# Kernel tuning notes

Measured on AMD Instinct MI355X. Metric: run time of the kernel, lower is better.

Reference implementation:

```python
import jax, jax.numpy as jnp
import numpy as np
from jax import lax

B, C, H, W = 2, 64, 384, 384
WS = 8; NH = 4; HD = C // NH; S = WS * WS  # 64 tokens per window
EPS = 1e-5


def setup_inputs() -> dict:
    key = jax.random.key(0)
    ks = jax.random.split(key, 16)
    def n(k, shape, s=0.02):
        return jax.random.normal(k, shape, jnp.float32) * s
    return {
        "x": jax.random.normal(ks[0], (B, C, H, W), jnp.float32),
        "norm1_w": jnp.ones((C,), jnp.float32), "norm1_b": jnp.zeros((C,), jnp.float32),
        "qkv_w": n(ks[1], (3 * C, C)), "qkv_b": jnp.zeros((3 * C,), jnp.float32),
        "pos_bias": n(ks[2], (1, S, NH, NH), 0.01),  # faithful: bias over (tokens, heads, heads)
        "out_w": n(ks[3], (C, C)), "out_b": jnp.zeros((C,), jnp.float32),
        "convp_w": n(ks[4], (C, C)), "convp_b": jnp.zeros((C,), jnp.float32),
        "pw1_w": n(ks[5], (C, C, 1)), "pw1_b": jnp.zeros((C,), jnp.float32),
        "dw1_w": n(ks[6], (C, 1, 3)), "dw1_b": jnp.zeros((C,), jnp.float32),
        "tok_w": n(ks[7], (C, C)), "tok_b": jnp.zeros((C,), jnp.float32),
        "norm2_w": jnp.ones((C,), jnp.float32), "norm2_b": jnp.zeros((C,), jnp.float32),
        "leff_pw_w": n(ks[8], (C, C, 1, 1)),
        "leff_dw_w": n(ks[9], (C, 1, 3, 3)), "leff_dw_b": jnp.zeros((C,), jnp.float32),
        "fc1_w": n(ks[10], (4 * C, C)), "fc1_b": jnp.zeros((4 * C,), jnp.float32),
        "fc2_w": n(ks[11], (C, 4 * C)), "fc2_b": jnp.zeros((C,), jnp.float32),
    }


def _ln_c(x, w, b):
    # channel-wise LayerNorm (Restormer 'WithBias') on (B,C,H,W), biased variance
    mu = x.mean(axis=1, keepdims=True)
    var = ((x - mu) ** 2).mean(axis=1, keepdims=True)
    return (x - mu) / jnp.sqrt(var + EPS) * w[None, :, None, None] + b[None, :, None, None]


def _lin(x, w, b):
    return x @ w.T + b


def _win_part(x):
    # (B,C,H,W) -> (B*nw, S, C); H,W divisible by WS so pad is a no-op
    b = x.shape[0]
    x = x.reshape(b, C, H // WS, WS, W // WS, WS)
    return x.transpose(0, 2, 4, 3, 5, 1).reshape(-1, S, C)


def _win_merge(wins):
    b = wins.shape[0] // ((H // WS) * (W // WS))
    x = wins.reshape(b, H // WS, W // WS, WS, WS, C)
    return x.transpose(0, 5, 1, 3, 2, 4).reshape(b, C, H, W)


def _remsa(xw, qkv_w, qkv_b, pos_bias, out_w, out_b, convp_w, convp_b,
           pw1_w, pw1_b, dw1_w, dw1_b, tok_w, tok_b):
    bw = xw.shape[0]
    qkv = _lin(xw, qkv_w, qkv_b).reshape(bw, S, NH, 3 * HD)
    q, k, v = jnp.split(qkv, 3, axis=-1)  # each (bw, S, NH, HD)
    # Faithful to source: NO head transpose -> attention mixes across the heads axis
    scores = jnp.einsum('bshd,bsgd->bshg', q, k) * (HD ** -0.5) + pos_bias  # (bw,S,NH,NH)
    attn = jax.nn.softmax(scores, axis=-1)
    ao = jnp.einsum('bshg,bsgd->bshd', attn, v).reshape(bw, S, C)
    ao = _lin(ao, out_w, out_b)
    # convolutional branch
    xc = _lin(xw, convp_w, convp_b).transpose(0, 2, 1)  # (bw, C, S)
    xc = jnp.einsum('bcs,oc->bos', xc, pw1_w[:, :, 0]) + pw1_b[None, :, None]  # 1x1 conv1d
    xc = lax.conv_general_dilated(xc, dw1_w, (1,), 'SAME', feature_group_count=C,
                                  dimension_numbers=('NCH', 'OIH', 'NCH')) + dw1_b[None, :, None]
    xc = _lin(xc.transpose(0, 2, 1), tok_w, tok_b)
    return ao + xc


def _leff(x, pw_w, dw_w, dw_b, fc1_w, fc1_b, fc2_w, fc2_b):
    b = x.shape[0]
    y = lax.conv_general_dilated(x, pw_w, (1, 1), 'SAME',
                                 dimension_numbers=('NCHW', 'OIHW', 'NCHW'))  # 1x1, no bias
    y = lax.conv_general_dilated(y, dw_w, (1, 1), 'SAME', feature_group_count=C,
                                 dimension_numbers=('NCHW', 'OIHW', 'NCHW')) + dw_b[None, :, None, None]
    y = y.transpose(0, 2, 3, 1).reshape(b, H * W, C)
    y = jax.nn.gelu(_lin(y, fc1_w, fc1_b), approximate=False)
    y = _lin(y, fc2_w, fc2_b)
    return y.reshape(b, H, W, C).transpose(0, 3, 1, 2)


def reference(x, norm1_w, norm1_b, qkv_w, qkv_b, pos_bias, out_w, out_b,
              convp_w, convp_b, pw1_w, pw1_b, dw1_w, dw1_b, tok_w, tok_b,
              norm2_w, norm2_b, leff_pw_w, leff_dw_w, leff_dw_b,
              fc1_w, fc1_b, fc2_w, fc2_b):
    xw = _win_part(_ln_c(x, norm1_w, norm1_b))
    r = _win_merge(_remsa(xw, qkv_w, qkv_b, pos_bias, out_w, out_b, convp_w, convp_b,
                          pw1_w, pw1_b, dw1_w, dw1_b, tok_w, tok_b))
    x = x + r
    x = x + _leff(_ln_c(x, norm2_w, norm2_b), leff_pw_w, leff_dw_w, leff_dw_b,
                  fc1_w, fc1_b, fc2_w, fc2_b)
    return x
```

## Files before the change

kernel.cpp:

```cpp
#include <hip/hip_runtime.h>
#include <hip/hip_bf16.h>
#include <math.h>

#define Bn 2
#define Cc 64
#define Hh 384
#define Ww 384
#define HW (Hh*Ww)
#define Tt (Bn*HW)

using f32x4  = __attribute__((ext_vector_type(4))) float;
using bf16x8 = __attribute__((ext_vector_type(8))) short;


__device__ __forceinline__ unsigned short f2bf_u(float f) {
  return __builtin_bit_cast(unsigned short, __float2bfloat16(f));
}
__device__ __forceinline__ float bf2f(unsigned short u) {
  union { unsigned u; float f; } v; v.u = ((unsigned)u) << 16;
  return v.f;
}
__device__ __forceinline__ float gelu_exact(float v) {
  return 0.5f * v * (1.0f + erff(v * 0.70710678118654752f));
}

__device__ __forceinline__ void stage_wtile(char* dst, const float* __restrict__ g, int rs, int tid) {
#pragma unroll
  for (int half = 0; half < 2; ++half) {
    int q = tid + half * 256;
    int row = q >> 3, ks = q & 7;
    const float* gp = g + (long)row * rs + ks * 8;
    float4 a = *(const float4*)gp;
    float4 b = *(const float4*)(gp + 4);
    bf16x8 o;
    o[0] = (short)f2bf_u(a.x); o[1] = (short)f2bf_u(a.y);
    o[2] = (short)f2bf_u(a.z); o[3] = (short)f2bf_u(a.w);
    o[4] = (short)f2bf_u(b.x); o[5] = (short)f2bf_u(b.y);
    o[6] = (short)f2bf_u(b.z); o[7] = (short)f2bf_u(b.w);
    *(bf16x8*)(dst + row * 128 + ((ks * 16) ^ ((row & 7) << 4))) = o;
  }
}

__device__ __forceinline__ void mfma64(const char* sA, const char* sB, int wid, int lane, f32x4 acc[4]) {
  const int r = lane & 15, kq = lane >> 4;
#pragma unroll
  for (int kh = 0; kh < 2; ++kh) {
    const int arow = wid * 16 + r;
    bf16x8 af = *(const bf16x8*)(sA + arow * 128 + ((kh * 64 + kq * 16) ^ ((arow & 7) << 4)));
#pragma unroll
    for (int nt = 0; nt < 4; ++nt) {
      const int brow = nt * 16 + r;
      bf16x8 bfv = *(const bf16x8*)(sB + brow * 128 + ((kh * 64 + kq * 16) ^ ((brow & 7) << 4)));
      acc[nt] = __builtin_amdgcn_mfma_f32_16x16x32_bf16(af, bfv, acc[nt], 0, 0, 0);
    }
  }
}


__global__ __launch_bounds__(512, 4) void kA(
    const float* __restrict__ x, unsigned short* __restrict__ x1g, unsigned short* __restrict__ yg,
    const float* __restrict__ n1w, const float* __restrict__ n1b,
    const float* __restrict__ qkvw, const float* __restrict__ qkvb,
    const float* __restrict__ posb,
    const float* __restrict__ outw, const float* __restrict__ outb,
    const float* __restrict__ cpw, const float* __restrict__ cpb,
    const float* __restrict__ pw1w, const float* __restrict__ pw1b,
    const float* __restrict__ dw1w, const float* __restrict__ dw1b,
    const float* __restrict__ tokw, const float* __restrict__ tokb,
    const float* __restrict__ n2w, const float* __restrict__ n2b,
    const float* __restrict__ lpw) {
  __shared__ char sX[16384];
  __shared__ char sW0[8192];
  __shared__ char sW1[8192];
  __shared__ char sQ[49152];

  const int tid = threadIdx.x;
  const int lane = tid & 63, wid = tid >> 6;
  const int fr = lane & 15, kq = lane >> 4;
  const int rtok = tid & 127;
  const int cpar = tid >> 7;
  const int c0own = cpar * 16;
  const int iy = rtok >> 4, ix = rtok & 15;
  const int blk = blockIdx.x;
  const int b = blk / 1152;
  const int rr = blk - b * 1152;
  const int wy = rr / 24, wxp = rr - (rr / 24) * 24;
  const int h0 = wy * 8, w0 = wxp * 16;
  const long ibase = (long)b * HW;

  float4 wr0, wr1;
  const int wrow = tid >> 3, wc0 = (tid & 7) * 8;
  auto WLOAD = [&](const float* g) {
    const float* p = g + (long)wrow * 64 + wc0;
    wr0 = *(const float4*)p; wr1 = *(const float4*)(p + 4);
  };
  auto WSTORE = [&](char* dst) {
    bf16x8 o;
    o[0]=(short)f2bf_u(wr0.x); o[1]=(short)f2bf_u(wr0.y); o[2]=(short)f2bf_u(wr0.z); o[3]=(short)f2bf_u(wr0.w);
    o[4]=(short)f2bf_u(wr1.x); o[5]=(short)f2bf_u(wr1.y); o[6]=(short)f2bf_u(wr1.z); o[7]=(short)f2bf_u(wr1.w);
    *(bf16x8*)(dst + wrow * 128 + ((2 * wc0) ^ ((wrow & 7) << 4))) = o;
  };

  WLOAD(cpw);
  const float* xb = x + ((long)(b * 64 + c0own)) * HW + (long)(h0 + iy) * Ww + (w0 + ix);
  float vx[16]; float s0 = 0.f, s1 = 0.f;
#pragma unroll
  for (int k = 0; k < 16; ++k) {
    float v = xb[(long)k * HW];
    vx[k] = v; s0 += v; s1 += v * v;
  }
  float* ps1 = (float*)sW1;
  ps1[cpar * 128 + rtok] = s0;
  ps1[512 + cpar * 128 + rtok] = s1;
  WSTORE(sW0); WLOAD(pw1w);
  __syncthreads();
  if (tid < 128) {
    float s = ps1[tid] + ps1[128 + tid] + ps1[256 + tid] + ps1[384 + tid];
    float q = ps1[512 + tid] + ps1[640 + tid] + ps1[768 + tid] + ps1[896 + tid];
    float m = s * (1.f / 64.f);
    ps1[1024 + tid] = m; ps1[1152 + tid] = rsqrtf(q * (1.f / 64.f) - m * m + 1e-5f);
  }
  __syncthreads();
  {
    float m = ps1[1024 + rtok], ri = ps1[1152 + rtok];
    const int swz = (rtok & 7) << 4;
#pragma unroll
    for (int q8 = 0; q8 < 2; ++q8) {
      bf16x8 o;
#pragma unroll
      for (int j = 0; j < 8; ++j) {
        int c = c0own + q8 * 8 + j;
        o[j] = (short)f2bf_u((vx[q8 * 8 + j] - m) * ri * n1w[c] + n1b[c]);
      }
      *(bf16x8*)(sX + rtok * 128 + ((c0own * 2 + q8 * 16) ^ swz)) = o;
    }
  }
  __syncthreads();

  f32x4 acc[4], res[4];
  auto ZERO = [&](f32x4 a[4]) {
#pragma unroll
    for (int nt = 0; nt < 4; ++nt) a[nt] = (f32x4){0.f, 0.f, 0.f, 0.f};
  };
  auto GEMM = [&](const char* A, const char* W, f32x4 a[4]) {
#pragma unroll
    for (int kh = 0; kh < 2; ++kh) {
      const int arow = wid * 16 + fr;
      bf16x8 af = *(const bf16x8*)(A + arow * 128 + ((kh * 64 + kq * 16) ^ ((arow & 7) << 4)));
#pragma unroll
      for (int nt = 0; nt < 4; ++nt) {
        const int brow = nt * 16 + fr;
        bf16x8 bv = *(const bf16x8*)(W + brow * 128 + ((kh * 64 + kq * 16) ^ ((brow & 7) << 4)));
        a[nt] = __builtin_amdgcn_mfma_f32_16x16x32_bf16(af, bv, a[nt], 0, 0, 0);
      }
    }
  };
  auto EPI = [&](char* dst, f32x4 a[4], const float* bias) {
    const int rb = wid * 16 + kq * 4;
#pragma unroll
    for (int nt = 0; nt < 4; ++nt) {
      const int col = nt * 16 + fr;
      const float bv = bias[col];
#pragma unroll
      for (int reg = 0; reg < 4; ++reg) {
        const int row = rb + reg;
        *(unsigned short*)(dst + row * 128 + ((2 * col) ^ ((row & 7) << 4))) = f2bf_u(a[nt][reg] + bv);
      }
    }
  };
  char* t0 = sQ; char* t1 = sQ + 16384; char* t2 = sQ + 32768;
  float* sQf = (float*)sQ;

  ZERO(acc); GEMM(sX, sW0, acc); EPI(t0, acc, cpb);
  WSTORE(sW1); WLOAD(tokw);
  __syncthreads();
  ZERO(acc); GEMM(t0, sW1, acc); EPI(t1, acc, pw1b);
  WSTORE(sW0); WLOAD(qkvw);
  __syncthreads();
  {
    const int c = tid & 63, tq = tid >> 6;
    const int wl = tq >> 2, chunk = tq & 3;
    float wv0 = dw1w[c * 3], wv1 = dw1w[c * 3 + 1], wv2 = dw1w[c * 3 + 2], bia = dw1b[c];
#pragma unroll
    for (int k = 0; k < 16; ++k) {
      int s = chunk * 16 + k;
      int r0 = ((s >> 3) << 4) + wl * 8 + (s & 7);
      float v = bia + bf2f(*(const unsigned short*)(t1 + r0 * 128 + ((2 * c) ^ ((r0 & 7) << 4)))) * wv1;
      if (s > 0) {
        int rm = (((s - 1) >> 3) << 4) + wl * 8 + ((s - 1) & 7);
        v += bf2f(*(const unsigned short*)(t1 + rm * 128 + ((2 * c) ^ ((rm & 7) << 4)))) * wv0;
      }
      if (s < 63) {
        int rp = (((s + 1) >> 3) << 4) + wl * 8 + ((s + 1) & 7);
        v += bf2f(*(const unsigned short*)(t1 + rp * 128 + ((2 * c) ^ ((rp & 7) << 4)))) * wv2;
      }
      *(unsigned short*)(t0 + r0 * 128 + ((2 * c) ^ ((r0 & 7) << 4))) = f2bf_u(v);
    }
  }
  WSTORE(sW1); WLOAD(qkvw + 4096);
  __syncthreads();
  ZERO(res); GEMM(t0, sW0, res);
  __syncthreads();
  ZERO(acc); GEMM(sX, sW1, acc); EPI(t0, acc, qkvb);
  WSTORE(sW0); WLOAD(qkvw + 8192);
  __syncthreads();
  ZERO(acc); GEMM(sX, sW0, acc); EPI(t1, acc, qkvb + 64);
  WSTORE(sW1); WLOAD(outw);
  __syncthreads();
  ZERO(acc); GEMM(sX, sW1, acc); EPI(t2, acc, qkvb + 128);
  WSTORE(sW0); WLOAD(lpw);
  __syncthreads();
  {
    const int r = rtok;
    const int h = cpar;
    const int s = ((r >> 4) << 3) + (r & 7);
    const int swz = (r & 7) << 4;
    auto LD16 = [&](int gcol, float* o) {
      const char* base = sQ + ((gcol >> 6) * 16384) + r * 128;
      int c0 = (gcol & 63) * 2;
      bf16x8 u = *(const bf16x8*)(base + (c0 ^ swz));
      bf16x8 w2_ = *(const bf16x8*)(base + ((c0 + 16) ^ swz));
#pragma unroll
      for (int j = 0; j < 8; ++j) {
        o[j] = bf2f((unsigned short)u[j]); o[8 + j] = bf2f((unsigned short)w2_[j]);
      }
    };
    float q0[16];
    LD16(48 * h, q0);
    float sc[4];
#pragma unroll
    for (int g = 0; g < 4; ++g) {
      float kk[16]; LD16(48 * g + 16, kk);
      float a = 0.f;
#pragma unroll
      for (int d = 0; d < 16; ++d) a += q0[d] * kk[d];
      sc[g] = a * 0.25f + posb[s * 16 + h * 4 + g];
    }
    float m = fmaxf(fmaxf(sc[0], sc[1]), fmaxf(sc[2], sc[3]));
    float e[4]; float tsum = 0.f;
#pragma unroll
    for (int g = 0; g < 4; ++g) { e[g] = __expf(sc[g] - m); tsum += e[g]; }
    float inv = 1.f / tsum;
    float ao[16];
#pragma unroll
    for (int d = 0; d < 16; ++d) ao[d] = 0.f;
#pragma unroll
    for (int g = 0; g < 4; ++g) {
      float vv[16]; LD16(48 * g + 32, vv);
#pragma unroll
      for (int d = 0; d < 16; ++d) ao[d] += e[g] * vv[d];
    }
    bf16x8 o1, o2;
#pragma unroll
    for (int j = 0; j < 8; ++j) { o1[j] = (short)f2bf_u(ao[j] * inv); o2[j] = (short)f2bf_u(ao[8 + j] * inv); }
    *(bf16x8*)(sX + r * 128 + ((h * 32) ^ swz)) = o1;
    *(bf16x8*)(sX + r * 128 + ((h * 32 + 16) ^ swz)) = o2;
  }
  WSTORE(sW1);
  __syncthreads();
  GEMM(sX, sW0, res);
  {
    const int rb = wid * 16 + kq * 4;
#pragma unroll
    for (int nt = 0; nt < 4; ++nt) {
      const int col = nt * 16 + fr;
      const float ob = outb[col] + tokb[col];
#pragma unroll
      for (int reg = 0; reg < 4; ++reg)
        sQf[(rb + reg) * 67 + col] = res[nt][reg] + ob;
    }
  }
  __syncthreads();
  float* ps2 = (float*)sW0;
  {
    float ss0 = 0.f, ss1 = 0.f;
#pragma unroll
    for (int k = 0; k < 16; ++k) {
      float v = sQf[rtok * 67 + c0own + k] + vx[k];
      vx[k] = v; ss0 += v; ss1 += v * v;
    }
    ps2[cpar * 128 + rtok] = ss0;
    ps2[512 + cpar * 128 + rtok] = ss1;
  }
  __syncthreads();
  if (tid < 128) {
    float s = ps2[tid] + ps2[128 + tid] + ps2[256 + tid] + ps2[384 + tid];
    float q = ps2[512 + tid] + ps2[640 + tid] + ps2[768 + tid] + ps2[896 + tid];
    float m = s * (1.f / 64.f);
    ps2[1024 + tid] = m; ps2[1152 + tid] = rsqrtf(q * (1.f / 64.f) - m * m + 1e-5f);
  }
  __syncthreads();
  {
    float m = ps2[1024 + rtok], ri = ps2[1152 + rtok];
    const int swz = (rtok & 7) << 4;
    long t = ibase + (long)(h0 + iy) * Ww + (w0 + ix);
#pragma unroll
    for (int q8 = 0; q8 < 2; ++q8) {
      bf16x8 xo, no;
#pragma unroll
      for (int j = 0; j < 8; ++j) {
        int c = c0own + q8 * 8 + j;
        float v = vx[q8 * 8 + j];
        xo[j] = (short)f2bf_u(v);
        no[j] = (short)f2bf_u((v - m) * ri * n2w[c] + n2b[c]);
      }
      *(bf16x8*)((char*)x1g + t * 128 + (c0own + q8 * 8) * 2) = xo;
      *(bf16x8*)(sX + rtok * 128 + ((c0own * 2 + q8 * 16) ^ swz)) = no;
    }
  }
  __syncthreads();
  ZERO(acc); GEMM(sX, sW1, acc);
  {
    const int rb = wid * 16 + kq * 4;
#pragma unroll
    for (int nt = 0; nt < 4; ++nt) {
      const int col = nt * 16 + fr;
#pragma unroll
      for (int reg = 0; reg < 4; ++reg)
        sQf[(rb + reg) * 67 + col] = acc[nt][reg];
    }
  }
  __syncthreads();
  {
    long t = ibase + (long)(h0 + iy) * Ww + (w0 + ix);
#pragma unroll
    for (int q8 = 0; q8 < 2; ++q8) {
      bf16x8 o;
#pragma unroll
      for (int j = 0; j < 8; ++j)
        o[j] = (short)f2bf_u(sQf[rtok * 67 + c0own + q8 * 8 + j]);
      *(bf16x8*)((char*)yg + t * 128 + (c0own + q8 * 8) * 2) = o;
    }
  }
}


__global__ __launch_bounds__(256, 3) void kB(
    const unsigned short* __restrict__ yg, const unsigned short* __restrict__ x1g,
    float* __restrict__ out,
    const float* __restrict__ ldw, const float* __restrict__ ldb,
    const float* __restrict__ f1w, const float* __restrict__ f1b,
    const float* __restrict__ f2w, const float* __restrict__ f2b) {
  __shared__ char sZ0[8192];
  __shared__ char sZ1[8192];
  __shared__ char U[33792];
  __shared__ float wtab[640];

  const int tid = threadIdx.x;
  const int lane = tid & 63, wid = tid >> 6;
  const int bid = blockIdx.x;
  const int b = bid / 1152;
  const int r2 = bid - b * 1152;
  const int hp = r2 / 6, wseg = r2 - (r2 / 6) * 6;
  const int h0 = hp * 2, w0 = wseg * 64;
  const long ibase = (long)b * HW;
  const int cbase = lane & 15;
  const int rbase = wid * 16 + (lane >> 4) * 4;

  unsigned short x1r[2][4][4];
#pragma unroll
  for (int t = 0; t < 2; ++t) {
    const long p0t = ibase + (long)(h0 + t) * Ww + w0;
#pragma unroll
    for (int nt = 0; nt < 4; ++nt) {
      int col = nt * 16 + cbase;
#pragma unroll
      for (int reg = 0; reg < 4; ++reg)
        x1r[t][nt][reg] = x1g[(p0t + rbase + reg) * 64 + col];
    }
  }

#pragma unroll
  for (int it = 0; it < 3; ++it) {
    int idx = it * 256 + tid;
    if (idx < 576) wtab[idx] = ldw[(idx & 63) * 9 + (idx >> 6)];
    else if (idx < 640) wtab[idx] = ldb[idx - 576];
  }

  for (int it = 0; it < 9; ++it) {
    int idx = it * 256 + tid;
    if (idx >= 2112) break;
    int hr = idx / 528;
    int rq = idx - hr * 528;
    int px = rq >> 3, c8 = rq & 7;
    int h = h0 - 1 + hr, w = w0 - 1 + px;
    uint4 v = make_uint4(0, 0, 0, 0);
    if (h >= 0 && h < Hh && w >= 0 && w < Ww) {
      long t = ibase + (long)h * Ww + w;
      v = *(const uint4*)((const char*)yg + t * 128 + c8 * 16);
    }
    *(uint4*)(U + (hr * 66 + px) * 128 + c8 * 16) = v;
  }
  __syncthreads();

  {
    const int c8 = tid & 7, c0 = c8 * 8;
#pragma unroll
    for (int it = 0; it < 4; ++it) {
      int task = it * 256 + tid;
      int r = task >> 9;
      int px = (task >> 3) & 63;
      float a8[8];
#pragma unroll
      for (int j = 0; j < 8; ++j) a8[j] = wtab[576 + c0 + j];
#pragma unroll
      for (int dy = 0; dy < 3; ++dy)
#pragma unroll
        for (int dx = 0; dx < 3; ++dx) {
          bf16x8 v = *(const bf16x8*)(U + ((r + dy) * 66 + px + dx) * 128 + c8 * 16);
          const float* wk = wtab + (dy * 3 + dx) * 64 + c0;
#pragma unroll
          for (int j = 0; j < 8; ++j) a8[j] += bf2f((unsigned short)v[j]) * wk[j];
        }
      char* sZ = r ? sZ1 : sZ0;
      bf16x8 o;
#pragma unroll
      for (int j = 0; j < 8; ++j) o[j] = (short)f2bf_u(a8[j]);
      *(bf16x8*)(sZ + px * 128 + ((c8 * 16) ^ ((px & 7) << 4))) = o;
    }
  }
  __syncthreads();

  char* sW  = U;
  char* sH0 = U + 8192;
  char* sH1 = U + 16384;
  f32x4 res0[4], res1[4];
#pragma unroll
  for (int nt = 0; nt < 4; ++nt) { res0[nt] = (f32x4){0.f,0.f,0.f,0.f}; res1[nt] = (f32x4){0.f,0.f,0.f,0.f}; }

  for (int jc = 0; jc < 4; ++jc) {
    stage_wtile(sW, f1w + jc * 4096, 64, tid);
    __syncthreads();
#pragma unroll
    for (int t = 0; t < 2; ++t) {
      f32x4 acc[4];
#pragma unroll
      for (int nt = 0; nt < 4; ++nt) acc[nt] = (f32x4){0.f,0.f,0.f,0.f};
      mfma64(t ? sZ1 : sZ0, sW, wid, lane, acc);
      char* sH = t ? sH1 : sH0;
#pragma unroll
      for (int nt = 0; nt < 4; ++nt) {
        const int col = nt * 16 + cbase;
        const float bv = f1b[jc * 64 + col];
#pragma unroll
        for (int reg = 0; reg < 4; ++reg) {
          const int row = rbase + reg;
          *(unsigned short*)(sH + row * 128 + ((col * 2) ^ ((row & 7) << 4))) =
              f2bf_u(gelu_exact(acc[nt][reg] + bv));
        }
      }
    }
    __syncthreads();
    stage_wtile(sW, f2w + jc * 64, 256, tid);
    __syncthreads();
    mfma64(sH0, sW, wid, lane, res0);
    mfma64(sH1, sW, wid, lane, res1);
    __syncthreads();
  }

  float* sO = (float*)U;
#pragma unroll
  for (int t = 0; t < 2; ++t) {
    const f32x4* res = t ? res1 : res0;
#pragma unroll
    for (int nt = 0; nt < 4; ++nt) {
      const int col = nt * 16 + cbase;
      const float bv = f2b[col];
#pragma unroll
      for (int reg = 0; reg < 4; ++reg) {
        const int row = rbase + reg;
        sO[row * 65 + col] = res[nt][reg] + bv + bf2f(x1r[t][nt][reg]);
      }
    }
    __syncthreads();
#pragma unroll
    for (int it = 0; it < 16; ++it) {
      int c = it * 4 + (tid >> 6);
      int wo = tid & 63;
      out[(((long)(b * Cc + c)) * Hh + (h0 + t)) * Ww + w0 + wo] = sO[wo * 65 + c];
    }
    __syncthreads();
  }
}


extern "C" void kernel_launch(void* const* d_in, const int* in_sizes, int n_in,
                              void* d_out, int out_size, void* d_ws, size_t ws_size,
                              hipStream_t stream) {
  const float* x    = (const float*)d_in[0];
  const float* n1w  = (const float*)d_in[1];
  const float* n1b  = (const float*)d_in[2];
  const float* qkvw = (const float*)d_in[3];
  const float* qkvb = (const float*)d_in[4];
  const float* posb = (const float*)d_in[5];
  const float* outw = (const float*)d_in[6];
  const float* outb = (const float*)d_in[7];
  const float* cpw  = (const float*)d_in[8];
  const float* cpb  = (const float*)d_in[9];
  const float* pw1w = (const float*)d_in[10];
  const float* pw1b = (const float*)d_in[11];
  const float* dw1w = (const float*)d_in[12];
  const float* dw1b = (const float*)d_in[13];
  const float* tokw = (const float*)d_in[14];
  const float* tokb = (const float*)d_in[15];
  const float* n2w  = (const float*)d_in[16];
  const float* n2b  = (const float*)d_in[17];
  const float* lpw  = (const float*)d_in[18];
  const float* ldw  = (const float*)d_in[19];
  const float* ldb  = (const float*)d_in[20];
  const float* f1w  = (const float*)d_in[21];
  const float* f1b  = (const float*)d_in[22];
  const float* f2w  = (const float*)d_in[23];
  const float* f2b  = (const float*)d_in[24];
  float* out = (float*)d_out;

  unsigned short* x1 = (unsigned short*)d_ws;
  unsigned short* y  = x1 + (size_t)Tt * 64;

  kA<<<dim3(2304), dim3(512), 0, stream>>>(x, x1, y, n1w, n1b, qkvw, qkvb, posb,
                                           outw, outb, cpw, cpb, pw1w, pw1b,
                                           dw1w, dw1b, tokw, tokb, n2w, n2b, lpw);
  kB<<<dim3(2304), dim3(256), 0, stream>>>(y, x1, out, ldw, ldb, f1w, f1b, f2w, f2b);
}
```

Baseline: 198.2 us.

## Use wave shuffles for LayerNorm stats and register-block the depthwise conv

The thread-to-token mapping is changed so that the four channel-quarter threads of each token sit in the same wavefront. Both LayerNorm reductions then use xor shuffles instead of shared-memory partial sums and two extra barriers each. Separately, the 3x3 depthwise conv has each thread compute 4 adjacent pixels, reusing 6 loaded bf16 columns per row so that LDS reads and weight loads are amortised. The price is more registers per thread, which could lower occupancy, and the remapping touches the attention head assignment as well.

```diff
diff --git a/kernel.cpp b/kernel.cpp
--- a/kernel.cpp
+++ b/kernel.cpp
@@ -77,10 +77,9 @@
   const int tid = threadIdx.x;
   const int lane = tid & 63, wid = tid >> 6;
   const int fr = lane & 15, kq = lane >> 4;
-  const int rtok = tid & 127;
-  const int cpar = tid >> 7;
-  const int c0own = cpar * 16;
-  const int iy = rtok >> 4, ix = rtok & 15;
+  const int rtok = wid * 16 + fr;
+  const int c0own = kq * 16;
+  const int iy = wid, ix = fr;
   const int blk = blockIdx.x;
   const int b = blk / 1152;
   const int rr = blk - b * 1152;
@@ -109,20 +108,11 @@
     float v = xb[(long)k * HW];
     vx[k] = v; s0 += v; s1 += v * v;
   }
-  float* ps1 = (float*)sW1;
-  ps1[cpar * 128 + rtok] = s0;
-  ps1[512 + cpar * 128 + rtok] = s1;
-  WSTORE(sW0); WLOAD(pw1w);
-  __syncthreads();
-  if (tid < 128) {
-    float s = ps1[tid] + ps1[128 + tid] + ps1[256 + tid] + ps1[384 + tid];
-    float q = ps1[512 + tid] + ps1[640 + tid] + ps1[768 + tid] + ps1[896 + tid];
-    float m = s * (1.f / 64.f);
-    ps1[1024 + tid] = m; ps1[1152 + tid] = rsqrtf(q * (1.f / 64.f) - m * m + 1e-5f);
-  }
-  __syncthreads();
-  {
-    float m = ps1[1024 + rtok], ri = ps1[1152 + rtok];
+  s0 += __shfl_xor(s0, 16); s0 += __shfl_xor(s0, 32);
+  s1 += __shfl_xor(s1, 16); s1 += __shfl_xor(s1, 32);
+  {
+    float m = s0 * (1.f / 64.f);
+    float ri = rsqrtf(s1 * (1.f / 64.f) - m * m + 1e-5f);
     const int swz = (rtok & 7) << 4;
 #pragma unroll
     for (int q8 = 0; q8 < 2; ++q8) {
@@ -135,6 +125,7 @@
       *(bf16x8*)(sX + rtok * 128 + ((c0own * 2 + q8 * 16) ^ swz)) = o;
     }
   }
+  WSTORE(sW0); WLOAD(pw1w);
   __syncthreads();
 
   f32x4 acc[4], res[4];
@@ -212,7 +203,7 @@
   __syncthreads();
   {
     const int r = rtok;
-    const int h = cpar;
+    const int h = kq;
     const int s = ((r >> 4) << 3) + (r & 7);
     const int swz = (r & 7) << 4;
     auto LD16 = [&](int gcol, float* o) {
@@ -271,7 +262,6 @@
     }
   }
   __syncthreads();
-  float* ps2 = (float*)sW0;
   {
     float ss0 = 0.f, ss1 = 0.f;
 #pragma unroll
@@ -279,19 +269,10 @@
       float v = sQf[rtok * 67 + c0own + k] + vx[k];
       vx[k] = v; ss0 += v; ss1 += v * v;
     }
-    ps2[cpar * 128 + rtok] = ss0;
-    ps2[512 + cpar * 128 + rtok] = ss1;
-  }
-  __syncthreads();
-  if (tid < 128) {
-    float s = ps2[tid] + ps2[128 + tid] + ps2[256 + tid] + ps2[384 + tid];
-    float q = ps2[512 + tid] + ps2[640 + tid] + ps2[768 + tid] + ps2[896 + tid];
-    float m = s * (1.f / 64.f);
-    ps2[1024 + tid] = m; ps2[1152 + tid] = rsqrtf(q * (1.f / 64.f) - m * m + 1e-5f);
-  }
-  __syncthreads();
-  {
-    float m = ps2[1024 + rtok], ri = ps2[1152 + rtok];
+    ss0 += __shfl_xor(ss0, 16); ss0 += __shfl_xor(ss0, 32);
+    ss1 += __shfl_xor(ss1, 16); ss1 += __shfl_xor(ss1, 32);
+    float m = ss0 * (1.f / 64.f);
+    float ri = rsqrtf(ss1 * (1.f / 64.f) - m * m + 1e-5f);
     const int swz = (rtok & 7) << 4;
     long t = ibase + (long)(h0 + iy) * Ww + (w0 + ix);
 #pragma unroll
@@ -395,27 +376,41 @@
 
   {
     const int c8 = tid & 7, c0 = c8 * 8;
-#pragma unroll
-    for (int it = 0; it < 4; ++it) {
-      int task = it * 256 + tid;
-      int r = task >> 9;
-      int px = (task >> 3) & 63;
-      float a8[8];
-#pragma unroll
-      for (int j = 0; j < 8; ++j) a8[j] = wtab[576 + c0 + j];
-#pragma unroll
-      for (int dy = 0; dy < 3; ++dy)
-#pragma unroll
-        for (int dx = 0; dx < 3; ++dx) {
-          bf16x8 v = *(const bf16x8*)(U + ((r + dy) * 66 + px + dx) * 128 + c8 * 16);
-          const float* wk = wtab + (dy * 3 + dx) * 64 + c0;
-#pragma unroll
-          for (int j = 0; j < 8; ++j) a8[j] += bf2f((unsigned short)v[j]) * wk[j];
-        }
-      char* sZ = r ? sZ1 : sZ0;
+    const int r = tid >> 7;
+    const int px0 = ((tid >> 3) & 15) * 4;
+    float a[4][8];
+#pragma unroll
+    for (int p = 0; p < 4; ++p)
+#pragma unroll
+      for (int j = 0; j < 8; ++j) a[p][j] = wtab[576 + c0 + j];
+#pragma unroll
+    for (int dy = 0; dy < 3; ++dy) {
+      float fu[6][8];
+#pragma unroll
+      for (int i = 0; i < 6; ++i) {
+        bf16x8 u = *(const bf16x8*)(U + ((r + dy) * 66 + px0 + i) * 128 + c8 * 16);
+#pragma unroll
+        for (int j = 0; j < 8; ++j) fu[i][j] = bf2f((unsigned short)u[j]);
+      }
+#pragma unroll
+      for (int dx = 0; dx < 3; ++dx) {
+        const float* wk = wtab + (dy * 3 + dx) * 64 + c0;
+        float w8[8];
+#pragma unroll
+        for (int j = 0; j < 8; ++j) w8[j] = wk[j];
+#pragma unroll
+        for (int p = 0; p < 4; ++p)
+#pragma unroll
+          for (int j = 0; j < 8; ++j) a[p][j] += fu[p + dx][j] * w8[j];
+      }
+    }
+    char* sZ = r ? sZ1 : sZ0;
+#pragma unroll
+    for (int p = 0; p < 4; ++p) {
+      int px = px0 + p;
       bf16x8 o;
 #pragma unroll
-      for (int j = 0; j < 8; ++j) o[j] = (short)f2bf_u(a8[j]);
+      for (int j = 0; j < 8; ++j) o[j] = (short)f2bf_u(a[p][j]);
       *(bf16x8*)(sZ + px * 128 + ((c8 * 16) ^ ((px & 7) << 4))) = o;
     }
   }
```

Result: slower. 226.5 us (+14.3%).
